# Kernel tuning notes

Measured on AMD Instinct MI355X. Metric: run time of the kernel, lower is better.

Reference implementation:

```python
import jax, jax.numpy as jnp
import numpy as np

ENT_TYPE_SIZE = 9
INNER_DIM = 64
NEG_INF = 1e12


def _rope_interleaved(x, cos_pos, sin_pos):
    # x: (B, S, H, D); rotate interleaved pairs: (x0,x1)->(x0*c - x1*s, x1*c + x0*s)
    x2 = jnp.stack([-x[..., 1::2], x[..., ::2]], axis=-1).reshape(x.shape)
    return x * cos_pos + x2 * sin_pos


def setup_inputs() -> dict:
    key = jax.random.key(0)
    k1, k2 = jax.random.split(key)
    B, S, H = 16, 512, 768
    out_dim = ENT_TYPE_SIZE * INNER_DIM * 2  # 1152
    last_hidden_state = jax.random.normal(k1, (B, S, H), dtype=jnp.float32)
    attention_mask = jnp.ones((B, S), dtype=jnp.float32)
    W_dense = jax.random.normal(k2, (H, out_dim), dtype=jnp.float32) * (1.0 / np.sqrt(H))
    b_dense = jnp.zeros((out_dim,), dtype=jnp.float32)
    return {
        "last_hidden_state": last_hidden_state,
        "attention_mask": attention_mask,
        "W_dense": W_dense,
        "b_dense": b_dense,
    }


def reference(last_hidden_state, attention_mask, W_dense, b_dense):
    B, S, H = last_hidden_state.shape
    ent, inner = ENT_TYPE_SIZE, INNER_DIM

    # dense projection then split into per-entity-type q/k vectors
    proj = last_hidden_state @ W_dense + b_dense            # (B, S, ent*2*inner)
    proj = proj.reshape(B, S, ent, 2 * inner)
    qw, kw = proj[..., :inner], proj[..., inner:]           # (B, S, ent, inner)

    # inline RoPE, interleaved sin/cos layout per sinusoidal_position_embedding
    pos = jnp.arange(S, dtype=jnp.float32)[:, None]         # (S, 1)
    idx = jnp.arange(inner // 2, dtype=jnp.float32)
    freqs = pos * jnp.power(10000.0, -2.0 * idx / inner)    # (S, inner/2)
    cos_pos = jnp.repeat(jnp.cos(freqs), 2, axis=-1)[None, :, None, :]  # (1,S,1,inner)
    sin_pos = jnp.repeat(jnp.sin(freqs), 2, axis=-1)[None, :, None, :]
    qw = _rope_interleaved(qw, cos_pos, sin_pos)
    kw = _rope_interleaved(kw, cos_pos, sin_pos)

    # pairwise span scores
    logits = jnp.einsum('bmhd,bnhd->bhmn', qw, kw)          # (B, ent, S, S)

    # padding mask on key positions (canonical GlobalPointer masking)
    pad = attention_mask[:, None, None, :]                  # (B,1,1,S)
    logits = logits * pad - (1.0 - pad) * NEG_INF

    # strict lower triangle masked out (only spans with start <= end)
    tril = jnp.tril(jnp.ones((S, S), dtype=logits.dtype), -1)
    logits = logits - tril * NEG_INF

    return logits / (inner ** 0.5)
```

## Files before the change

kernel.cpp:

```cpp
#include <hip/hip_runtime.h>
#include <hip/hip_bf16.h>
#include <cstdint>

typedef __bf16 bf8 __attribute__((ext_vector_type(8)));
typedef __bf16 bf4 __attribute__((ext_vector_type(4)));
typedef float  f4  __attribute__((ext_vector_type(4)));

typedef const void __attribute__((address_space(1)))* as1_cvp;
typedef void       __attribute__((address_space(3)))* as3_vp;

#define NEG_INF_F 1000000000000.0f

__device__ __forceinline__ void lds_load16(const __bf16* g, __bf16* l) {
    __builtin_amdgcn_global_load_lds((as1_cvp)g, (as3_vp)l, 16, 0, 0);
}

__device__ __forceinline__ void gemm_tile_core(
    const __bf16* __restrict__ Atile, const __bf16* __restrict__ Btile,
    int lda, int ldb, int Ktot,
    __bf16* sA, __bf16* sB, f4 acc[4][4])
{
    const int t    = threadIdx.x;
    const int wave = t >> 6;
    const int lane = t & 63;
    const int quad = lane >> 4;
    const int m16  = lane & 15;
    const int wm   = (wave >> 1) * 64;
    const int wn   = (wave & 1) * 64;

    for (int k0 = 0; k0 < Ktot; k0 += 32) {
        __syncthreads();
#pragma unroll
        for (int i = 0; i < 2; ++i) {
            const int f   = i * 256 + t;
            const int row = f >> 2;
            const int ch  = (f & 3) * 8;
            lds_load16(Atile + (size_t)row * lda + k0 + ch,
                       sA + (i * 256 + wave * 64) * 8);
            lds_load16(Btile + (size_t)row * ldb + k0 + ch,
                       sB + (i * 256 + wave * 64) * 8);
        }
        __syncthreads();

        bf8 af[4], bfr[4];
#pragma unroll
        for (int mi = 0; mi < 4; ++mi)
            af[mi] = *(const bf8*)(sA + (wm + mi * 16 + m16) * 32 + quad * 8);
#pragma unroll
        for (int ni = 0; ni < 4; ++ni)
            bfr[ni] = *(const bf8*)(sB + (wn + ni * 16 + m16) * 32 + quad * 8);
#pragma unroll
        for (int mi = 0; mi < 4; ++mi)
#pragma unroll
            for (int ni = 0; ni < 4; ++ni)
                acc[mi][ni] = __builtin_amdgcn_mfma_f32_16x16x32_bf16(
                    af[mi], bfr[ni], acc[mi][ni], 0, 0, 0);
    }
}

__global__ __launch_bounds__(256) void cast_a_kernel(
    const float* __restrict__ in, __bf16* __restrict__ out, int n4)
{
    int idx = blockIdx.x * 256 + threadIdx.x;
    if (idx < n4) {
        const float4 v = reinterpret_cast<const float4*>(in)[idx];
        bf4 o = { (__bf16)v.x, (__bf16)v.y, (__bf16)v.z, (__bf16)v.w };
        reinterpret_cast<bf4*>(out)[idx] = o;
    }
}

__global__ __launch_bounds__(256) void transpose_w_kernel(
    const float* __restrict__ W, __bf16* __restrict__ Wt)
{
    __shared__ __bf16 tile[32][33];
    const int n0 = blockIdx.x * 32;
    const int k0 = blockIdx.y * 32;
    const int tx = threadIdx.x & 31;
    const int ty = threadIdx.x >> 5;
#pragma unroll
    for (int r = 0; r < 32; r += 8)
        tile[ty + r][tx] = (__bf16)W[(size_t)(k0 + ty + r) * 1152 + n0 + tx];
    __syncthreads();
#pragma unroll
    for (int r = 0; r < 32; r += 8)
        Wt[(size_t)(n0 + ty + r) * 768 + k0 + tx] = tile[tx][ty + r];
}

__global__ __launch_bounds__(256) void proj_rope_kernel(
    const __bf16* __restrict__ A,
    const __bf16* __restrict__ Wt,
    const float*  __restrict__ bias,
    __bf16* __restrict__ qbuf, __bf16* __restrict__ kbuf)
{
    __shared__ __bf16 sA[128 * 32];
    __shared__ __bf16 sB[128 * 32];
    f4 acc[4][4] = {};

    const int rowTile = blockIdx.y * 128;
    const int colTile = blockIdx.x * 128;
    gemm_tile_core(A + (size_t)rowTile * 768, Wt + (size_t)colTile * 768,
                   768, 768, 768, sA, sB, acc);

    const int t = threadIdx.x, wave = t >> 6, lane = t & 63;
    const int quad = lane >> 4, m16 = lane & 15;
    const int wm = (wave >> 1) * 64, wn = (wave & 1) * 64;

#pragma unroll
    for (int ni = 0; ni < 4; ++ni) {
        const int gc = colTile + wn + ni * 16 + m16;
        const float bv = bias[gc];
        const int e  = gc >> 7;
        const int d  = gc & 63;
        const int qk = (gc >> 6) & 1;
        const float theta = exp2f((float)(d >> 1) * -0.4152410118609203f);
        const float sgn = (d & 1) ? 1.0f : -1.0f;
        __bf16* dst = qk ? kbuf : qbuf;
#pragma unroll
        for (int mi = 0; mi < 4; ++mi) {
#pragma unroll
            for (int r = 0; r < 4; ++r) {
                const int gm = rowTile + wm + mi * 16 + quad * 4 + r;
                const int bb = gm >> 9;
                const int s  = gm & 511;
                float v = acc[mi][ni][r] + bv;
                float p = __shfl_xor(v, 1);
                float sn, cs;
                __sincosf((float)s * theta, &sn, &cs);
                float o = v * cs + sgn * p * sn;
                dst[(size_t)(((bb * 9 + e) * 512 + s)) * 64 + d] = (__bf16)o;
            }
        }
    }
}

__global__ __launch_bounds__(256) void logits_kernel(
    const __bf16* __restrict__ qbuf, const __bf16* __restrict__ kbuf,
    const float* __restrict__ amask, float* __restrict__ out)
{
    __shared__ __bf16 sA[128 * 32];
    __shared__ __bf16 sB[128 * 32];
    f4 acc[4][4] = {};

    const int be = blockIdx.y;
    const int b  = be / 9;
    const int rowTile = (blockIdx.x >> 2) * 128;
    const int colTile = (blockIdx.x & 3) * 128;
    const __bf16* Q  = qbuf + (size_t)be * 512 * 64;
    const __bf16* Kt = kbuf + (size_t)be * 512 * 64;
    gemm_tile_core(Q + (size_t)rowTile * 64, Kt + (size_t)colTile * 64,
                   64, 64, 64, sA, sB, acc);

    const int t = threadIdx.x, wave = t >> 6, lane = t & 63;
    const int quad = lane >> 4, m16 = lane & 15;
    const int wm = (wave >> 1) * 64, wn = (wave & 1) * 64;

#pragma unroll
    for (int ni = 0; ni < 4; ++ni) {
        const int n = colTile + wn + ni * 16 + m16;
        const float pad    = amask[b * 512 + n];
        const float padoff = (1.0f - pad) * NEG_INF_F;
#pragma unroll
        for (int mi = 0; mi < 4; ++mi) {
#pragma unroll
            for (int r = 0; r < 4; ++r) {
                const int m = rowTile + wm + mi * 16 + quad * 4 + r;
                float v = acc[mi][ni][r] * pad - padoff;
                if (n < m) v -= NEG_INF_F;
                out[((size_t)(be * 512 + m) << 9) + n] = v * 0.125f;
            }
        }
    }
}

extern "C" void kernel_launch(void* const* d_in, const int* in_sizes, int n_in,
                              void* d_out, int out_size, void* d_ws, size_t ws_size,
                              hipStream_t stream) {
    const float* lhs   = (const float*)d_in[0];
    const float* amask = (const float*)d_in[1];
    const float* W     = (const float*)d_in[2];
    const float* bias  = (const float*)d_in[3];
    float* out = (float*)d_out;

    char* ws = (char*)d_ws;
    __bf16* Abf = (__bf16*)ws;
    __bf16* Wt  = (__bf16*)(ws + 12582912);
    __bf16* qb  = (__bf16*)(ws + 14352384);
    __bf16* kb  = (__bf16*)(ws + 23789568);

    cast_a_kernel<<<6144, 256, 0, stream>>>(lhs, Abf, 1572864);
    transpose_w_kernel<<<dim3(36, 24), 256, 0, stream>>>(W, Wt);
    proj_rope_kernel<<<dim3(9, 64), 256, 0, stream>>>(Abf, Wt, bias, qb, kb);
    logits_kernel<<<dim3(16, 144), 256, 0, stream>>>(qb, kb, amask, out);
}
```

Measured before the change: 231.1 us.

## Keep Q tile resident and double-buffer K column tiles in logits kernel

Each logits block now owns a 128-row Q tile, loads it into LDS once, and loops over the four 128-column K tiles. The next K tile is prefetched into a second LDS buffer while the current one is multiplied and stored. This cuts redundant Q loads and block launch overhead and lets K loads overlap compute and output stores, with launch bounds asking for 3 blocks per CU. The trade-off is a grid four times smaller (576 blocks) and more LDS per block, which may lower parallelism for this store-bound kernel.

New measurement: 227.3 us. No clear change (-1.6%).

```diff
diff --git a/kernel.cpp b/kernel.cpp
--- a/kernel.cpp
+++ b/kernel.cpp
@@ -133,42 +133,91 @@
     }
 }
 
-__global__ __launch_bounds__(256) void logits_kernel(
+__global__ __launch_bounds__(256, 3) void logits_kernel(
     const __bf16* __restrict__ qbuf, const __bf16* __restrict__ kbuf,
     const float* __restrict__ amask, float* __restrict__ out)
 {
-    __shared__ __bf16 sA[128 * 32];
-    __shared__ __bf16 sB[128 * 32];
-    f4 acc[4][4] = {};
+    __shared__ __bf16 sQ[2 * 128 * 32];
+    __shared__ __bf16 sK[2][2 * 128 * 32];
+
+    const int t    = threadIdx.x;
+    const int wave = t >> 6;
+    const int lane = t & 63;
+    const int quad = lane >> 4;
+    const int m16  = lane & 15;
+    const int wm   = (wave >> 1) * 64;
+    const int wn   = (wave & 1) * 64;
 
     const int be = blockIdx.y;
     const int b  = be / 9;
-    const int rowTile = (blockIdx.x >> 2) * 128;
-    const int colTile = (blockIdx.x & 3) * 128;
-    const __bf16* Q  = qbuf + (size_t)be * 512 * 64;
-    const __bf16* Kt = kbuf + (size_t)be * 512 * 64;
-    gemm_tile_core(Q + (size_t)rowTile * 64, Kt + (size_t)colTile * 64,
-                   64, 64, 64, sA, sB, acc);
-
-    const int t = threadIdx.x, wave = t >> 6, lane = t & 63;
-    const int quad = lane >> 4, m16 = lane & 15;
-    const int wm = (wave >> 1) * 64, wn = (wave & 1) * 64;
-
-#pragma unroll
-    for (int ni = 0; ni < 4; ++ni) {
-        const int n = colTile + wn + ni * 16 + m16;
-        const float pad    = amask[b * 512 + n];
-        const float padoff = (1.0f - pad) * NEG_INF_F;
-#pragma unroll
-        for (int mi = 0; mi < 4; ++mi) {
-#pragma unroll
-            for (int r = 0; r < 4; ++r) {
-                const int m = rowTile + wm + mi * 16 + quad * 4 + r;
-                float v = acc[mi][ni][r] * pad - padoff;
-                if (n < m) v -= NEG_INF_F;
-                out[((size_t)(be * 512 + m) << 9) + n] = v * 0.125f;
+    const int rowTile = blockIdx.x * 128;
+    const __bf16* Qg = qbuf + (size_t)be * 512 * 64 + (size_t)rowTile * 64;
+    const __bf16* Kg = kbuf + (size_t)be * 512 * 64;
+
+#pragma unroll
+    for (int i = 0; i < 4; ++i) {
+        const int l = i * 256 + t;
+        const int p = l >> 9;
+        const int r = (l >> 2) & 127;
+        const int j = l & 3;
+        const int g = r * 8 + p * 4 + j;
+        lds_load16(Qg + g * 8, sQ + (i * 256 + wave * 64) * 8);
+        lds_load16(Kg + g * 8, sK[0] + (i * 256 + wave * 64) * 8);
+    }
+    __syncthreads();
+
+    for (int c = 0; c < 4; ++c) {
+        if (c < 3) {
+            const __bf16* Kc = Kg + (size_t)(c + 1) * 128 * 64;
+            __bf16* dstb = sK[(c + 1) & 1];
+#pragma unroll
+            for (int i = 0; i < 4; ++i) {
+                const int l = i * 256 + t;
+                const int p = l >> 9;
+                const int r = (l >> 2) & 127;
+                const int j = l & 3;
+                const int g = r * 8 + p * 4 + j;
+                lds_load16(Kc + g * 8, dstb + (i * 256 + wave * 64) * 8);
             }
         }
+
+        const __bf16* sKc = sK[c & 1];
+        f4 acc[4][4] = {};
+#pragma unroll
+        for (int kp = 0; kp < 2; ++kp) {
+            bf8 af[4], bfr[4];
+#pragma unroll
+            for (int mi = 0; mi < 4; ++mi)
+                af[mi] = *(const bf8*)(sQ + kp * 4096 + (wm + mi * 16 + m16) * 32 + quad * 8);
+#pragma unroll
+            for (int ni = 0; ni < 4; ++ni)
+                bfr[ni] = *(const bf8*)(sKc + kp * 4096 + (wn + ni * 16 + m16) * 32 + quad * 8);
+#pragma unroll
+            for (int mi = 0; mi < 4; ++mi)
+#pragma unroll
+                for (int ni = 0; ni < 4; ++ni)
+                    acc[mi][ni] = __builtin_amdgcn_mfma_f32_16x16x32_bf16(
+                        af[mi], bfr[ni], acc[mi][ni], 0, 0, 0);
+        }
+
+        const int colTile = c * 128;
+#pragma unroll
+        for (int ni = 0; ni < 4; ++ni) {
+            const int n = colTile + wn + ni * 16 + m16;
+            const float pad    = amask[b * 512 + n];
+            const float padoff = (1.0f - pad) * NEG_INF_F;
+#pragma unroll
+            for (int mi = 0; mi < 4; ++mi) {
+#pragma unroll
+                for (int r = 0; r < 4; ++r) {
+                    const int m = rowTile + wm + mi * 16 + quad * 4 + r;
+                    float v = acc[mi][ni][r] * pad - padoff;
+                    if (n < m) v -= NEG_INF_F;
+                    out[((size_t)(be * 512 + m) << 9) + n] = v * 0.125f;
+                }
+            }
+        }
+        __syncthreads();
     }
 }
 
@@ -190,5 +239,5 @@
     cast_a_kernel<<<6144, 256, 0, stream>>>(lhs, Abf, 1572864);
     transpose_w_kernel<<<dim3(36, 24), 256, 0, stream>>>(W, Wt);
     proj_rope_kernel<<<dim3(9, 64), 256, 0, stream>>>(Abf, Wt, bias, qb, kb);
-    logits_kernel<<<dim3(16, 144), 256, 0, stream>>>(qb, kb, amask, out);
-}
+    logits_kernel<<<dim3(4, 144), 256, 0, stream>>>(qb, kb, amask, out);
+}
```
